# Performance work log

Measured on AMD Instinct MI355X. Metric: run time of the kernel, lower is better.

## Reference

```python
import jax, jax.numpy as jnp
import numpy as np

NEG_SLOPE = 0.01  # PyTorch LeakyReLU default

def lrelu(x):
    return jnp.where(x >= 0, x, NEG_SLOPE * x)

def setup_inputs() -> dict:
    key = jax.random.key(0)
    ks = jax.random.split(key, 16)
    d, nu, ni, nr = 64, 50000, 25000, 400000
    s = 1.0 / np.sqrt(d)
    f = jnp.float32
    return {
        "Xu": jax.random.normal(ks[0], (nu, d), f),
        "Xi": jax.random.normal(ks[1], (ni, d), f),
        "Wsrc": jax.random.normal(ks[2], (d, d), f) * s,
        "bsrc": jnp.zeros((d,), f),
        "Wdst": jax.random.normal(ks[3], (d, d), f) * s,
        "bdst": jnp.zeros((d,), f),
        "watt_rep": jax.random.normal(ks[4], (d,), f) * s,
        "batt_rep": jnp.zeros((), f),
        "Wo": jax.random.normal(ks[5], (d, d), f) * s,
        "bo": jnp.zeros((d,), f),
        "Wu": jax.random.normal(ks[6], (d, d), f) * s,
        "bu": jnp.zeros((d,), f),
        "watt_agg": jax.random.normal(ks[7], (d,), f) * s,
        "batt_agg": jnp.zeros((), f),
        "pref_user": jax.random.normal(ks[8], (nu, d), f),
        "pref_item": jax.random.normal(ks[9], (ni, d), f),
        "r_user": jax.random.randint(ks[10], (400000,), 0, nu),
        "r_item": jax.random.randint(ks[11], (400000,), 0, ni),
    }

def reference(Xu, Xi, Wsrc, bsrc, Wdst, bdst, watt_rep, batt_rep,
              Wo, bo, Wu, bu, watt_agg, batt_agg,
              pref_user, pref_item, r_user, r_item):
    nu, ni = Xu.shape[0], Xi.shape[0]
    # ---- ReviewRepresentationConv ----
    # Each review has exactly one user edge and one item edge, so per-etype
    # mean over edges is a gather; cross-type 'mean' averages the two types.
    agg = 0.5 * (Xu[r_user] + Xi[r_item])                 # [R, d]
    hs_u = Xu @ Wsrc + bsrc                               # src_w_a(x)
    hs_i = Xi @ Wsrc + bsrc
    hd_r = agg @ Wdst + bdst                              # dst_w_a(agg)
    # raw exp attention (module uses torch.exp, not stable edge_softmax here)
    a_u = jnp.exp(lrelu(hs_u[r_user] + hd_r) @ watt_rep + batt_rep)  # [R]
    a_i = jnp.exp(lrelu(hs_i[r_item] + hd_r) @ watt_rep + batt_rep)
    denom = a_u + a_i                                     # e_div_v normalizer
    h_rev = (a_u / denom)[:, None] * Xu[r_user] + (a_i / denom)[:, None] * Xi[r_item]
    # ---- ReviewAggregatorConv ----
    h_o = h_rev @ Wo + bo                                 # w_o(src review feats)

    def agg_side(npid_emb, dst, n_dst):
        z = lrelu(h_o + npid_emb @ Wu + bu)               # u_add_e then LeakyReLU
        a = z @ watt_agg + batt_agg                       # [R] attention logits
        m = jax.ops.segment_max(a, dst, num_segments=n_dst)
        e = jnp.exp(a - m[dst])                           # stable edge_softmax
        ssum = jax.ops.segment_sum(e, dst, num_segments=n_dst)
        w = e / ssum[dst]
        # u_mul_e + sum scatter-reduce
        return jax.ops.segment_sum(h_rev * w[:, None], dst, num_segments=n_dst)

    out_user = agg_side(pref_item[r_item], r_user, nu)    # [nu, d]
    out_item = agg_side(pref_user[r_user], r_item, ni)    # [ni, d]
    return jnp.concatenate([out_user, out_item], axis=0)  # [nu+ni, d]
```

## Files before the change

kernel.cpp:

```cpp
#include <hip/hip_runtime.h>
#include <hip/hip_fp16.h>
#include <math.h>

#define D 64
#define EPB 1024

typedef _Float16 f16x8 __attribute__((ext_vector_type(8)));
typedef _Float16 f16x4 __attribute__((ext_vector_type(4)));
typedef float f32x4 __attribute__((ext_vector_type(4)));

__device__ __forceinline__ float lrelu(float x) { return fmaxf(x, 0.f) + 0.01f * fminf(x, 0.f); }

__global__ void k_count(const int* __restrict__ ru, const int* __restrict__ ri,
                        int* __restrict__ cnt_u, int* __restrict__ cnt_i, int R) {
    int r = blockIdx.x * blockDim.x + threadIdx.x;
    if (r >= R) return;
    atomicAdd(&cnt_u[ru[r]], 1);
    atomicAdd(&cnt_i[ri[r]], 1);
}

__global__ void k_fill_u(const int* __restrict__ ru, const int* __restrict__ ri,
                         int* __restrict__ cur_u, int2* __restrict__ edges, int R) {
    int r = blockIdx.x * blockDim.x + threadIdx.x;
    if (r >= R) return;
    int u = ru[r], it = ri[r];
    int j = atomicAdd(&cur_u[u], 1);
    edges[j] = make_int2(u, it);
}

__global__ __launch_bounds__(256) void k_nodes_mfma(
    const float* __restrict__ Xu, const float* __restrict__ Pu, int nu, int ntu,
    const float* __restrict__ Xi_, const float* __restrict__ Pi, int ni, int nti,
    const float* __restrict__ Wsrc, const float* __restrict__ bsrc,
    const float* __restrict__ Wdst, const float* __restrict__ bdst,
    const float* __restrict__ Wo,   const float* __restrict__ bo,
    const float* __restrict__ Wu,   const float* __restrict__ bu,
    __half* __restrict__ packU, __half* __restrict__ Xuh,
    __half* __restrict__ packI, __half* __restrict__ Xih) {
    __shared__ __half sD[4][16][72];
    __shared__ float sb[4][64];
    int tid = threadIdx.x;
    int lane = tid & 63, w = tid >> 6;
    int col = lane & 15, kg = lane >> 4;

    {
        int c = tid & 63, m = tid >> 6;
        const float* bp = (m == 0) ? bsrc : (m == 1) ? bdst : (m == 2) ? bo : bu;
        sb[m][c] = bp[c];
    }
    const float* W = (w == 0) ? Wsrc : (w == 1) ? Wdst : (w == 2) ? Wo : Wu;
    f16x8 Bf[2][4];
#pragma unroll
    for (int kt = 0; kt < 2; ++kt)
#pragma unroll
        for (int ct = 0; ct < 4; ++ct) {
            int c = ct * 16 + col;
            int k0 = kt * 32 + kg * 8;
            f16x8 b;
#pragma unroll
            for (int j = 0; j < 8; ++j) b[j] = (_Float16)W[(k0 + j) * 64 + c];
            Bf[kt][ct] = b;
        }
    __syncthreads();

    int T = ntu + nti;
    for (int tile = blockIdx.x; tile < T; tile += gridDim.x) {
        bool usr = tile < ntu;
        const float* X = usr ? Xu : Xi_;
        const float* P = usr ? Pu : Pi;
        __half* pack = usr ? packU : packI;
        __half* Xh = usr ? Xuh : Xih;
        int n = usr ? nu : ni;
        int nb = (usr ? tile : tile - ntu) * 16;

        int arow = nb + col; if (arow >= n) arow = n - 1;
        const float* src = (w == 3) ? P : X;
        const float4* rp0 = (const float4*)(src + (size_t)arow * 64 + kg * 8);
        const float4* rp1 = (const float4*)(src + (size_t)arow * 64 + 32 + kg * 8);
        float4 a0 = rp0[0], a1 = rp0[1];
        float4 a2 = rp1[0], a3 = rp1[1];
        f16x8 A0, A1;
        A0[0] = (_Float16)a0.x; A0[1] = (_Float16)a0.y; A0[2] = (_Float16)a0.z; A0[3] = (_Float16)a0.w;
        A0[4] = (_Float16)a1.x; A0[5] = (_Float16)a1.y; A0[6] = (_Float16)a1.z; A0[7] = (_Float16)a1.w;
        A1[0] = (_Float16)a2.x; A1[1] = (_Float16)a2.y; A1[2] = (_Float16)a2.z; A1[3] = (_Float16)a2.w;
        A1[4] = (_Float16)a3.x; A1[5] = (_Float16)a3.y; A1[6] = (_Float16)a3.z; A1[7] = (_Float16)a3.w;
        if (w == 0) {
            *(f16x8*)(Xh + (size_t)arow * 64 + kg * 8) = A0;
            *(f16x8*)(Xh + (size_t)arow * 64 + 32 + kg * 8) = A1;
        }
        f32x4 acc[4];
#pragma unroll
        for (int ct = 0; ct < 4; ++ct) {
            acc[ct] = (f32x4){0.f, 0.f, 0.f, 0.f};
            acc[ct] = __builtin_amdgcn_mfma_f32_16x16x32_f16(A0, Bf[0][ct], acc[ct], 0, 0, 0);
            acc[ct] = __builtin_amdgcn_mfma_f32_16x16x32_f16(A1, Bf[1][ct], acc[ct], 0, 0, 0);
        }
        __syncthreads();
#pragma unroll
        for (int ct = 0; ct < 4; ++ct)
#pragma unroll
            for (int jj = 0; jj < 4; ++jj)
                sD[w][kg * 4 + jj][ct * 16 + col] = __float2half(acc[ct][jj]);
        __syncthreads();
        int r = tid >> 4, c0 = (tid & 15) * 4;
        int node = nb + r;
        if (node < n) {
            __half* dst = pack + (size_t)node * 256;
            f16x4 v[4];
#pragma unroll
            for (int q = 0; q < 4; ++q) {
                int c = c0 + q;
                float hs = __half2float(sD[0][r][c]) + sb[0][c];
                float hds = 0.5f * (__half2float(sD[1][r][c]) + sb[1][c]);
                float ho = __half2float(sD[2][r][c]) + sb[2][c];
                float pw = __half2float(sD[3][r][c]) + sb[3][c];
                v[0][q] = (_Float16)(hs + hds);
                v[1][q] = (_Float16)hds;
                v[2][q] = (_Float16)ho;
                v[3][q] = (_Float16)pw;
            }
#pragma unroll
            for (int m = 0; m < 4; ++m)
                *(f16x4*)(dst + m * 64 + c0) = v[m];
        }
    }
}

__global__ __launch_bounds__(256, 1) void k_rev1(
    const int2* __restrict__ edges,
    const __half* __restrict__ packU, const __half* __restrict__ packI,
    const float4* __restrict__ watt_rep4,
    const float4* __restrict__ watt_agg4, const float* __restrict__ batt_agg,
    int* __restrict__ cur_i,
    float4* __restrict__ pay_su, float4* __restrict__ pay_si,
    int R) {
    int tid = threadIdx.x;
    int lane = tid & 63;
    int f = lane & 7;
    int j = blockIdx.x * 32 + (tid >> 6) * 8 + (lane >> 3);
    if (j >= R) return;
    int2 e = edges[j];
    const __half* pu = packU + (size_t)e.x * 256 + f * 8;
    const __half* pi = packI + (size_t)e.y * 256 + f * 8;
    f16x8 f0u = *(const f16x8*)(pu);
    f16x8 hdu = *(const f16x8*)(pu + 64);
    f16x8 hou = *(const f16x8*)(pu + 128);
    f16x8 pwu = *(const f16x8*)(pu + 192);
    f16x8 f0i = *(const f16x8*)(pi);
    f16x8 hdi = *(const f16x8*)(pi + 64);
    f16x8 hoi = *(const f16x8*)(pi + 128);
    f16x8 pwi = *(const f16x8*)(pi + 192);

    f16x8 xu = f0u + hdi;
    f16x8 xi = f0i + hdu;
    float4 wrA = watt_rep4[f * 2], wrB = watt_rep4[f * 2 + 1];
    float tu =
        lrelu((float)xu[0]) * wrA.x + lrelu((float)xu[1]) * wrA.y +
        lrelu((float)xu[2]) * wrA.z + lrelu((float)xu[3]) * wrA.w +
        lrelu((float)xu[4]) * wrB.x + lrelu((float)xu[5]) * wrB.y +
        lrelu((float)xu[6]) * wrB.z + lrelu((float)xu[7]) * wrB.w;
    float ti =
        lrelu((float)xi[0]) * wrA.x + lrelu((float)xi[1]) * wrA.y +
        lrelu((float)xi[2]) * wrA.z + lrelu((float)xi[3]) * wrA.w +
        lrelu((float)xi[4]) * wrB.x + lrelu((float)xi[5]) * wrB.y +
        lrelu((float)xi[6]) * wrB.z + lrelu((float)xi[7]) * wrB.w;
#pragma unroll
    for (int o = 4; o; o >>= 1) {
        tu += __shfl_xor(tu, o, 64);
        ti += __shfl_xor(ti, o, 64);
    }
    float wu = 1.f / (1.f + __expf(ti - tu));
    float wi = 1.f - wu;
    float4 waA = watt_agg4[f * 2], waB = watt_agg4[f * 2 + 1];
    float zu = 0.f, zi = 0.f;
#pragma unroll
    for (int k = 0; k < 8; ++k) {
        float ho = wu * (float)hou[k] + wi * (float)hoi[k];
        float wa = (k < 4) ? ((const float*)&waA)[k] : ((const float*)&waB)[k - 4];
        zu += lrelu(ho + (float)pwi[k]) * wa;
        zi += lrelu(ho + (float)pwu[k]) * wa;
    }
#pragma unroll
    for (int o = 4; o; o >>= 1) {
        zu += __shfl_xor(zu, o, 64);
        zi += __shfl_xor(zi, o, 64);
    }
    if (f == 0) {
        float ba = batt_agg[0];
        pay_su[j] = make_float4(zu + ba, wu, __int_as_float(e.y), 0.f);
        int j2 = atomicAdd(&cur_i[e.y], 1);
        pay_si[j2] = make_float4(zi + ba, wu, __int_as_float(e.x), 0.f);
    }
}

__global__ __launch_bounds__(256) void k_scan_local(
    const int* __restrict__ cnt_u, int* __restrict__ off_u, int nu,
    const int* __restrict__ cnt_i, int* __restrict__ off_i, int ni,
    int* __restrict__ bsum, int Bu) {
    int b = blockIdx.x;
    const int* cnt; int* off; int n; int lb;
    if (b < Bu) { cnt = cnt_u; off = off_u; n = nu; lb = b; }
    else        { cnt = cnt_i; off = off_i; n = ni; lb = b - Bu; }
    int t = threadIdx.x;
    int idx0 = lb * EPB + t * 4;
    int v[4];
#pragma unroll
    for (int k = 0; k < 4; ++k) v[k] = (idx0 + k < n) ? cnt[idx0 + k] : 0;
    int s = v[0] + v[1] + v[2] + v[3];
    int lane = t & 63, w = t >> 6;
    int x = s;
#pragma unroll
    for (int o = 1; o < 64; o <<= 1) {
        int y = __shfl_up(x, o, 64);
        if (lane >= o) x += y;
    }
    __shared__ int wsum[4];
    if (lane == 63) wsum[w] = x;
    __syncthreads();
    int woff = 0;
    for (int j = 0; j < w; ++j) woff += wsum[j];
    int run = woff + x - s;
#pragma unroll
    for (int k = 0; k < 4; ++k) {
        if (idx0 + k < n) off[idx0 + k] = run;
        run += v[k];
    }
    if (t == 255) bsum[b] = woff + x;
}

__global__ __launch_bounds__(256) void k_scan_add(
    int* __restrict__ off_u, int* __restrict__ cur_u, int nu,
    int* __restrict__ off_i, int* __restrict__ cur_i, int ni,
    const int* __restrict__ bsum, int Bu, int Bi) {
    int b = blockIdx.x;
    int* off; int* cur; int n; int lb; const int* bs; int B;
    if (b < Bu) { off = off_u; cur = cur_u; n = nu; lb = b; bs = bsum; B = Bu; }
    else        { off = off_i; cur = cur_i; n = ni; lb = b - Bu; bs = bsum + Bu; B = Bi; }
    int boff = 0;
    for (int j = 0; j < lb; ++j) boff += bs[j];
    int idx0 = lb * EPB + threadIdx.x * 4;
#pragma unroll
    for (int k = 0; k < 4; ++k) {
        int idx = idx0 + k;
        if (idx < n) {
            int vv = off[idx] + boff;
            off[idx] = vv;
            cur[idx] = vv;
        }
    }
    if (lb == B - 1 && threadIdx.x == 0) off[n] = boff + bs[lb];
}

__global__ __launch_bounds__(256, 1) void k_agg(
    const int* __restrict__ off_u, const int* __restrict__ off_i,
    const float4* __restrict__ pay_su, const float4* __restrict__ pay_si,
    const float* __restrict__ Xu, const float* __restrict__ Xi,
    const __half* __restrict__ Xuh, const __half* __restrict__ Xih,
    float* __restrict__ out, int nu, int ntot) {
    int tid = threadIdx.x;
    int lane = tid & 63;
    int idx = blockIdx.x * 4 + (tid >> 6);
    if (idx >= ntot) return;
    bool user = idx < nu;
    int d = user ? idx : idx - nu;
    const int*    offp = user ? off_u : off_i;
    const float4* pay  = user ? pay_su : pay_si;
    const float*  Xown = user ? Xu : Xi;
    const __half* Xoth = user ? Xih : Xuh;
    int s = offp[d], e = offp[d + 1];
    if (s == e) { out[(size_t)idx * D + lane] = 0.f; return; }
    int g = lane >> 3;
    int l = lane & 7;
    float msum = 0.f, mcoef = 0.f;
    float acc[8] = {0.f, 0.f, 0.f, 0.f, 0.f, 0.f, 0.f, 0.f};
    for (int j = s + g; j < e; j += 8) {
        float4 p = pay[j];
        float ex = __expf(p.x);
        float wown = user ? p.y : 1.f - p.y;
        msum += ex;
        mcoef += ex * wown;
        float cv = ex * (1.f - wown);
        int o2 = __float_as_int(p.z);
        const __half2* row = (const __half2*)(Xoth + (size_t)o2 * D + 8 * l);
        float2 f0 = __half22float2(row[0]);
        float2 f1 = __half22float2(row[1]);
        float2 f2 = __half22float2(row[2]);
        float2 f3 = __half22float2(row[3]);
        acc[0] += cv * f0.x; acc[1] += cv * f0.y;
        acc[2] += cv * f1.x; acc[3] += cv * f1.y;
        acc[4] += cv * f2.x; acc[5] += cv * f2.y;
        acc[6] += cv * f3.x; acc[7] += cv * f3.y;
    }
#pragma unroll
    for (int o = 32; o >= 8; o >>= 1) {
        msum  += __shfl_xor(msum, o, 64);
        mcoef += __shfl_xor(mcoef, o, 64);
#pragma unroll
        for (int q = 0; q < 8; ++q) acc[q] += __shfl_xor(acc[q], o, 64);
    }
    if (g == 0) {
        float inv = 1.f / msum;
        const float4* xo = (const float4*)(Xown + (size_t)d * D + 8 * l);
        float4 x0 = xo[0], x1 = xo[1];
        float4 r0, r1;
        r0.x = (mcoef * x0.x + acc[0]) * inv;
        r0.y = (mcoef * x0.y + acc[1]) * inv;
        r0.z = (mcoef * x0.z + acc[2]) * inv;
        r0.w = (mcoef * x0.w + acc[3]) * inv;
        r1.x = (mcoef * x1.x + acc[4]) * inv;
        r1.y = (mcoef * x1.y + acc[5]) * inv;
        r1.z = (mcoef * x1.z + acc[6]) * inv;
        r1.w = (mcoef * x1.w + acc[7]) * inv;
        float4* op = (float4*)(out + (size_t)idx * D + 8 * l);
        op[0] = r0;
        op[1] = r1;
    }
}

extern "C" void kernel_launch(void* const* d_in, const int* in_sizes, int n_in,
                              void* d_out, int out_size, void* d_ws, size_t ws_size,
                              hipStream_t stream) {
    const float* Xu        = (const float*)d_in[0];
    const float* Xi        = (const float*)d_in[1];
    const float* Wsrc      = (const float*)d_in[2];
    const float* bsrc      = (const float*)d_in[3];
    const float* Wdst      = (const float*)d_in[4];
    const float* bdst      = (const float*)d_in[5];
    const float* watt_rep  = (const float*)d_in[6];
    const float* batt_rep  = (const float*)d_in[7];  (void)batt_rep;
    const float* Wo        = (const float*)d_in[8];
    const float* bo        = (const float*)d_in[9];
    const float* Wu        = (const float*)d_in[10];
    const float* bu        = (const float*)d_in[11];
    const float* watt_agg  = (const float*)d_in[12];
    const float* batt_agg  = (const float*)d_in[13];
    const float* pref_user = (const float*)d_in[14];
    const float* pref_item = (const float*)d_in[15];
    const int* r_user      = (const int*)d_in[16];
    const int* r_item      = (const int*)d_in[17];

    int nu = in_sizes[0] / D;
    int ni = in_sizes[1] / D;
    int R  = in_sizes[16];

    float* ws = (float*)d_ws;
    size_t off = 0;
    __half* packU = (__half*)(ws + off); off += (size_t)nu * D * 2;
    __half* packI = (__half*)(ws + off); off += (size_t)ni * D * 2;
    __half* Xuh = (__half*)(ws + off); off += (size_t)nu * D / 2;
    __half* Xih = (__half*)(ws + off); off += (size_t)ni * D / 2;
    float4* pay_su = (float4*)(ws + off); off += (size_t)R * 4;
    float4* pay_si = (float4*)(ws + off); off += (size_t)R * 4;
    int2* edges = (int2*)(ws + off); off += (size_t)R * 2;
    int* cnt_u = (int*)(ws + off); off += (size_t)nu;
    int* cnt_i = (int*)(ws + off); off += (size_t)ni;
    int* bsum  = (int*)(ws + off); off += 256;
    int* off_u = (int*)(ws + off); off += (size_t)nu + 1;
    int* off_i = (int*)(ws + off); off += (size_t)ni + 1;

    hipMemsetAsync(cnt_u, 0, (size_t)(nu + ni) * sizeof(int), stream);

    k_count<<<(R + 255) / 256, 256, 0, stream>>>(r_user, r_item, cnt_u, cnt_i, R);

    int Bu = (nu + EPB - 1) / EPB, Bi = (ni + EPB - 1) / EPB;
    k_scan_local<<<Bu + Bi, 256, 0, stream>>>(
        cnt_u, off_u, nu, cnt_i, off_i, ni, bsum, Bu);
    k_scan_add<<<Bu + Bi, 256, 0, stream>>>(
        off_u, cnt_u, nu, off_i, cnt_i, ni, bsum, Bu, Bi);

    k_fill_u<<<(R + 255) / 256, 256, 0, stream>>>(r_user, r_item, cnt_u, edges, R);

    int ntu = (nu + 15) / 16, nti = (ni + 15) / 16;
    k_nodes_mfma<<<1024, 256, 0, stream>>>(
        Xu, pref_user, nu, ntu, Xi, pref_item, ni, nti,
        Wsrc, bsrc, Wdst, bdst, Wo, bo, Wu, bu,
        packU, Xuh, packI, Xih);

    k_rev1<<<(R + 31) / 32, 256, 0, stream>>>(
        edges, packU, packI,
        (const float4*)watt_rep, (const float4*)watt_agg, batt_agg,
        cnt_i, pay_su, pay_si, R);

    int ntot = nu + ni;
    k_agg<<<(ntot + 3) / 4, 256, 0, stream>>>(
        off_u, off_i, pay_su, pay_si,
        Xu, Xi, Xuh, Xih, (float*)d_out, nu, ntot);
}
```

Measured before the change: 165.9 us.

## Fuse CSR build into one cooperative kernel and stage node tiles in LDS

Replaces the memset, count, two scan kernels and fill kernel with a single cooperative kernel that separates the phases with grid-wide syncs, removing four launches and their inter-kernel gaps. Separately, the node MFMA kernel now loads each 16-row tile of X and pref once into shared memory with coalesced float4 reads, instead of every wave reading rows from global memory. The trade-off is the cost of grid.sync barriers on a 512-block grid and an extra LDS round trip plus a block barrier per tile.

After: 369.7 us. +122.9%, slower.

```diff
diff --git a/kernel.cpp b/kernel.cpp
--- a/kernel.cpp
+++ b/kernel.cpp
@@ -1,6 +1,9 @@
 #include <hip/hip_runtime.h>
 #include <hip/hip_fp16.h>
+#include <hip/hip_cooperative_groups.h>
 #include <math.h>
+
+namespace cg = cooperative_groups;
 
 #define D 64
 #define EPB 1024
@@ -11,21 +14,78 @@
 
 __device__ __forceinline__ float lrelu(float x) { return fmaxf(x, 0.f) + 0.01f * fminf(x, 0.f); }
 
-__global__ void k_count(const int* __restrict__ ru, const int* __restrict__ ri,
-                        int* __restrict__ cnt_u, int* __restrict__ cnt_i, int R) {
-    int r = blockIdx.x * blockDim.x + threadIdx.x;
-    if (r >= R) return;
-    atomicAdd(&cnt_u[ru[r]], 1);
-    atomicAdd(&cnt_i[ri[r]], 1);
-}
-
-__global__ void k_fill_u(const int* __restrict__ ru, const int* __restrict__ ri,
-                         int* __restrict__ cur_u, int2* __restrict__ edges, int R) {
-    int r = blockIdx.x * blockDim.x + threadIdx.x;
-    if (r >= R) return;
-    int u = ru[r], it = ri[r];
-    int j = atomicAdd(&cur_u[u], 1);
-    edges[j] = make_int2(u, it);
+__global__ void k_build(const int* __restrict__ ru, const int* __restrict__ ri,
+                        int* __restrict__ cnt_u, int* __restrict__ cnt_i,
+                        int nu, int ni,
+                        int* __restrict__ off_u, int* __restrict__ off_i,
+                        int* __restrict__ bsum, int Bu, int Bi,
+                        int2* __restrict__ edges, int R) {
+    cg::grid_group grid = cg::this_grid();
+    __shared__ int wsum[4];
+    int tid = threadIdx.x, b = blockIdx.x;
+    int gsz = gridDim.x * blockDim.x;
+    int gid = b * blockDim.x + tid;
+
+    for (int j = gid; j < nu + ni; j += gsz) cnt_u[j] = 0;
+    grid.sync();
+    for (int r = gid; r < R; r += gsz) {
+        atomicAdd(&cnt_u[ru[r]], 1);
+        atomicAdd(&cnt_i[ri[r]], 1);
+    }
+    grid.sync();
+    if (b < Bu + Bi) {
+        const int* cnt; int* off; int n; int lb;
+        if (b < Bu) { cnt = cnt_u; off = off_u; n = nu; lb = b; }
+        else        { cnt = cnt_i; off = off_i; n = ni; lb = b - Bu; }
+        int idx0 = lb * EPB + tid * 4;
+        int v[4];
+#pragma unroll
+        for (int k = 0; k < 4; ++k) v[k] = (idx0 + k < n) ? cnt[idx0 + k] : 0;
+        int s = v[0] + v[1] + v[2] + v[3];
+        int lane = tid & 63, w = tid >> 6;
+        int x = s;
+#pragma unroll
+        for (int o = 1; o < 64; o <<= 1) {
+            int y = __shfl_up(x, o, 64);
+            if (lane >= o) x += y;
+        }
+        if (lane == 63) wsum[w] = x;
+        __syncthreads();
+        int woff = 0;
+        for (int j = 0; j < w; ++j) woff += wsum[j];
+        int run = woff + x - s;
+#pragma unroll
+        for (int k = 0; k < 4; ++k) {
+            if (idx0 + k < n) off[idx0 + k] = run;
+            run += v[k];
+        }
+        if (tid == 255) bsum[b] = woff + x;
+    }
+    grid.sync();
+    if (b < Bu + Bi) {
+        int* off; int* cur; int n; int lb; const int* bs; int B;
+        if (b < Bu) { off = off_u; cur = cnt_u; n = nu; lb = b; bs = bsum; B = Bu; }
+        else        { off = off_i; cur = cnt_i; n = ni; lb = b - Bu; bs = bsum + Bu; B = Bi; }
+        int boff = 0;
+        for (int j = 0; j < lb; ++j) boff += bs[j];
+        int idx0 = lb * EPB + tid * 4;
+#pragma unroll
+        for (int k = 0; k < 4; ++k) {
+            int idx = idx0 + k;
+            if (idx < n) {
+                int vv = off[idx] + boff;
+                off[idx] = vv;
+                cur[idx] = vv;
+            }
+        }
+        if (lb == B - 1 && tid == 0) off[n] = boff + bs[lb];
+    }
+    grid.sync();
+    for (int r = gid; r < R; r += gsz) {
+        int u = ru[r], it = ri[r];
+        int j = atomicAdd(&cnt_u[u], 1);
+        edges[j] = make_int2(u, it);
+    }
 }
 
 __global__ __launch_bounds__(256) void k_nodes_mfma(
@@ -37,6 +97,8 @@
     const float* __restrict__ Wu,   const float* __restrict__ bu,
     __half* __restrict__ packU, __half* __restrict__ Xuh,
     __half* __restrict__ packI, __half* __restrict__ Xih) {
+    __shared__ float sX[16 * 68];
+    __shared__ float sP[16 * 68];
     __shared__ __half sD[4][16][72];
     __shared__ float sb[4][64];
     int tid = threadIdx.x;
@@ -56,10 +118,10 @@
         for (int ct = 0; ct < 4; ++ct) {
             int c = ct * 16 + col;
             int k0 = kt * 32 + kg * 8;
-            f16x8 b;
-#pragma unroll
-            for (int j = 0; j < 8; ++j) b[j] = (_Float16)W[(k0 + j) * 64 + c];
-            Bf[kt][ct] = b;
+            f16x8 bfrag;
+#pragma unroll
+            for (int j = 0; j < 8; ++j) bfrag[j] = (_Float16)W[(k0 + j) * 64 + c];
+            Bf[kt][ct] = bfrag;
         }
     __syncthreads();
 
@@ -73,18 +135,26 @@
         int n = usr ? nu : ni;
         int nb = (usr ? tile : tile - ntu) * 16;
 
-        int arow = nb + col; if (arow >= n) arow = n - 1;
-        const float* src = (w == 3) ? P : X;
-        const float4* rp0 = (const float4*)(src + (size_t)arow * 64 + kg * 8);
-        const float4* rp1 = (const float4*)(src + (size_t)arow * 64 + 32 + kg * 8);
-        float4 a0 = rp0[0], a1 = rp0[1];
-        float4 a2 = rp1[0], a3 = rp1[1];
+        {
+            int rl = tid >> 4;
+            int c0s = (tid & 15) * 4;
+            int grow = nb + rl; if (grow >= n) grow = n - 1;
+            *(float4*)&sX[rl * 68 + c0s] = *(const float4*)(X + (size_t)grow * 64 + c0s);
+            *(float4*)&sP[rl * 68 + c0s] = *(const float4*)(P + (size_t)grow * 64 + c0s);
+        }
+        __syncthreads();
+        const float* srow = (w == 3) ? &sP[col * 68] : &sX[col * 68];
+        float4 a0 = *(const float4*)(srow + kg * 8);
+        float4 a1 = *(const float4*)(srow + kg * 8 + 4);
+        float4 a2 = *(const float4*)(srow + 32 + kg * 8);
+        float4 a3 = *(const float4*)(srow + 32 + kg * 8 + 4);
         f16x8 A0, A1;
         A0[0] = (_Float16)a0.x; A0[1] = (_Float16)a0.y; A0[2] = (_Float16)a0.z; A0[3] = (_Float16)a0.w;
         A0[4] = (_Float16)a1.x; A0[5] = (_Float16)a1.y; A0[6] = (_Float16)a1.z; A0[7] = (_Float16)a1.w;
         A1[0] = (_Float16)a2.x; A1[1] = (_Float16)a2.y; A1[2] = (_Float16)a2.z; A1[3] = (_Float16)a2.w;
         A1[4] = (_Float16)a3.x; A1[5] = (_Float16)a3.y; A1[6] = (_Float16)a3.z; A1[7] = (_Float16)a3.w;
         if (w == 0) {
+            int arow = nb + col; if (arow >= n) arow = n - 1;
             *(f16x8*)(Xh + (size_t)arow * 64 + kg * 8) = A0;
             *(f16x8*)(Xh + (size_t)arow * 64 + 32 + kg * 8) = A1;
         }
@@ -191,64 +261,6 @@
         int j2 = atomicAdd(&cur_i[e.y], 1);
         pay_si[j2] = make_float4(zi + ba, wu, __int_as_float(e.x), 0.f);
     }
-}
-
-__global__ __launch_bounds__(256) void k_scan_local(
-    const int* __restrict__ cnt_u, int* __restrict__ off_u, int nu,
-    const int* __restrict__ cnt_i, int* __restrict__ off_i, int ni,
-    int* __restrict__ bsum, int Bu) {
-    int b = blockIdx.x;
-    const int* cnt; int* off; int n; int lb;
-    if (b < Bu) { cnt = cnt_u; off = off_u; n = nu; lb = b; }
-    else        { cnt = cnt_i; off = off_i; n = ni; lb = b - Bu; }
-    int t = threadIdx.x;
-    int idx0 = lb * EPB + t * 4;
-    int v[4];
-#pragma unroll
-    for (int k = 0; k < 4; ++k) v[k] = (idx0 + k < n) ? cnt[idx0 + k] : 0;
-    int s = v[0] + v[1] + v[2] + v[3];
-    int lane = t & 63, w = t >> 6;
-    int x = s;
-#pragma unroll
-    for (int o = 1; o < 64; o <<= 1) {
-        int y = __shfl_up(x, o, 64);
-        if (lane >= o) x += y;
-    }
-    __shared__ int wsum[4];
-    if (lane == 63) wsum[w] = x;
-    __syncthreads();
-    int woff = 0;
-    for (int j = 0; j < w; ++j) woff += wsum[j];
-    int run = woff + x - s;
-#pragma unroll
-    for (int k = 0; k < 4; ++k) {
-        if (idx0 + k < n) off[idx0 + k] = run;
-        run += v[k];
-    }
-    if (t == 255) bsum[b] = woff + x;
-}
-
-__global__ __launch_bounds__(256) void k_scan_add(
-    int* __restrict__ off_u, int* __restrict__ cur_u, int nu,
-    int* __restrict__ off_i, int* __restrict__ cur_i, int ni,
-    const int* __restrict__ bsum, int Bu, int Bi) {
-    int b = blockIdx.x;
-    int* off; int* cur; int n; int lb; const int* bs; int B;
-    if (b < Bu) { off = off_u; cur = cur_u; n = nu; lb = b; bs = bsum; B = Bu; }
-    else        { off = off_i; cur = cur_i; n = ni; lb = b - Bu; bs = bsum + Bu; B = Bi; }
-    int boff = 0;
-    for (int j = 0; j < lb; ++j) boff += bs[j];
-    int idx0 = lb * EPB + threadIdx.x * 4;
-#pragma unroll
-    for (int k = 0; k < 4; ++k) {
-        int idx = idx0 + k;
-        if (idx < n) {
-            int vv = off[idx] + boff;
-            off[idx] = vv;
-            cur[idx] = vv;
-        }
-    }
-    if (lb == B - 1 && threadIdx.x == 0) off[n] = boff + bs[lb];
 }
 
 __global__ __launch_bounds__(256, 1) void k_agg(
@@ -358,17 +370,15 @@
     int* off_u = (int*)(ws + off); off += (size_t)nu + 1;
     int* off_i = (int*)(ws + off); off += (size_t)ni + 1;
 
-    hipMemsetAsync(cnt_u, 0, (size_t)(nu + ni) * sizeof(int), stream);
-
-    k_count<<<(R + 255) / 256, 256, 0, stream>>>(r_user, r_item, cnt_u, cnt_i, R);
-
     int Bu = (nu + EPB - 1) / EPB, Bi = (ni + EPB - 1) / EPB;
-    k_scan_local<<<Bu + Bi, 256, 0, stream>>>(
-        cnt_u, off_u, nu, cnt_i, off_i, ni, bsum, Bu);
-    k_scan_add<<<Bu + Bi, 256, 0, stream>>>(
-        off_u, cnt_u, nu, off_i, cnt_i, ni, bsum, Bu, Bi);
-
-    k_fill_u<<<(R + 255) / 256, 256, 0, stream>>>(r_user, r_item, cnt_u, edges, R);
+    {
+        void* args[] = {
+            (void*)&r_user, (void*)&r_item, (void*)&cnt_u, (void*)&cnt_i,
+            (void*)&nu, (void*)&ni, (void*)&off_u, (void*)&off_i,
+            (void*)&bsum, (void*)&Bu, (void*)&Bi, (void*)&edges, (void*)&R};
+        hipLaunchCooperativeKernel((void*)k_build, dim3(512), dim3(256),
+                                   args, 0, stream);
+    }
 
     int ntu = (nu + 15) / 16, nti = (ni + 15) / 16;
     k_nodes_mfma<<<1024, 256, 0, stream>>>(
```
